# Performance work log

Hardware: AMD Instinct MI355X
Metric: run time of the kernel (lower is better)

Reference implementation:

```python
import jax, jax.numpy as jnp
import numpy as np

B, T, I = 16384, 50, 5
H = 128
PRED_LEN = 12


def _uniform(key, shape, bound):
    return jax.random.uniform(key, shape, jnp.float32, -bound, bound)


def setup_inputs() -> dict:
    key = jax.random.key(0)
    ks = jax.random.split(key, 12)
    bound = 1.0 / np.sqrt(H)  # PyTorch LSTM/Linear default init
    return {
        "x": jax.random.normal(ks[0], (B, T, I), jnp.float32),
        "enc_Wih": _uniform(ks[1], (4 * H, I), bound),
        "enc_Whh": _uniform(ks[2], (4 * H, H), bound),
        "enc_bih": _uniform(ks[3], (4 * H,), bound),
        "enc_bhh": _uniform(ks[4], (4 * H,), bound),
        "dec_Wih": _uniform(ks[5], (4 * H, I), bound),
        "dec_Whh": _uniform(ks[6], (4 * H, H), bound),
        "dec_bih": _uniform(ks[7], (4 * H,), bound),
        "dec_bhh": _uniform(ks[8], (4 * H,), bound),
        "lin_W": _uniform(ks[9], (2, H), bound),
        "lin_b": _uniform(ks[10], (2,), bound),
    }


def _lstm_cell(x_t, h, c, Wih, Whh, bih, bhh):
    # PyTorch gate order: i, f, g, o
    gates = x_t @ Wih.T + h @ Whh.T + (bih + bhh)  # [B, 4H]
    i, f, g, o = jnp.split(gates, 4, axis=-1)
    i = jax.nn.sigmoid(i)
    f = jax.nn.sigmoid(f)
    g = jnp.tanh(g)
    o = jax.nn.sigmoid(o)
    c_new = f * c + i * g
    h_new = o * jnp.tanh(c_new)
    return h_new, c_new


def reference(x, enc_Wih, enc_Whh, enc_bih, enc_bhh,
              dec_Wih, dec_Whh, dec_bih, dec_bhh, lin_W, lin_b):
    b = x.shape[0]
    h0 = jnp.zeros((b, H), x.dtype)
    c0 = jnp.zeros((b, H), x.dtype)

    # ---- encoder LSTM over the history sequence ----
    def enc_step(carry, x_t):
        h, c = carry
        h, c = _lstm_cell(x_t, h, c, enc_Wih, enc_Whh, enc_bih, enc_bhh)
        return (h, c), None

    (h, c), _ = jax.lax.scan(enc_step, (h0, c0), jnp.swapaxes(x, 0, 1))

    static_context = x[:, -1, 2:]          # [B, I-2]
    last_velocity = x[:, -1, :2]           # [B, 2]
    dec_in0 = jnp.concatenate([last_velocity, static_context], axis=1)  # [B, I]

    def dec_step(carry, _):
        h, c, dec_in = carry
        h, c = _lstm_cell(dec_in, h, c, dec_Wih, dec_Whh, dec_bih, dec_bhh)
        pred = h @ lin_W.T + lin_b                      # [B, 2]
        dec_in = jnp.concatenate([pred, static_context], axis=1)
        return (h, c, dec_in), pred

    _, preds = jax.lax.scan(dec_step, (h, c, dec_in0), None, length=PRED_LEN)
    return jnp.swapaxes(preds, 0, 1)  # [B, pred_len, 2]
```

## Files before the change

kernel.cpp:

```cpp
#include <hip/hip_runtime.h>
#include <cstdint>

#define TT 50
#define II 5
#define PRED 12

typedef _Float16 f16;
typedef _Float16 f16x8 __attribute__((ext_vector_type(8)));
typedef float f32x4 __attribute__((ext_vector_type(4)));

#define K1 1.4426950408889634f
#define K2 2.8853900817779268f

__device__ __forceinline__ float cellact(float xi, float xf, float xg, float xo, float& c) {
    float ea = __builtin_amdgcn_exp2f(xi * -K1);
    float ef = __builtin_amdgcn_exp2f(xf * -K1);
    float eg = __builtin_amdgcn_exp2f(xg *  K2);
    float eo = __builtin_amdgcn_exp2f(xo * -K1);
    float a1 = 1.f + ea, a2 = 1.f + ef, a3 = eg + 1.f, a4 = eg - 1.f;
    float t1 = a1 * a3;
    float cn = fmaf(c, t1, a4 * a2) * __builtin_amdgcn_rcpf(t1 * a2);
    c = cn;
    float cc = fminf(fmaxf(cn, -15.f), 15.f);
    float ec = __builtin_amdgcn_exp2f(cc * K2);
    return (ec - 1.f) * __builtin_amdgcn_rcpf((1.f + eo) * (ec + 1.f));
}

__device__ __forceinline__ void load_weights(const float* __restrict__ Wih, const float* __restrict__ Whh,
                                             const float* __restrict__ bih, const float* __restrict__ bhh,
                                             f16x8 wr[4][5], int w, int cl, int q) {
    #pragma unroll
    for (int gs = 0; gs < 4; ++gs) {
        const int g = gs * 128 + w * 16 + cl;
        const float* row = Whh + g * 128 + q * 8;
        #pragma unroll
        for (int kc = 0; kc < 4; ++kc) {
            float4 a = *(const float4*)(row + kc * 32);
            float4 b = *(const float4*)(row + kc * 32 + 4);
            f16x8 r;
            r[0] = (f16)a.x; r[1] = (f16)a.y; r[2] = (f16)a.z; r[3] = (f16)a.w;
            r[4] = (f16)b.x; r[5] = (f16)b.y; r[6] = (f16)b.z; r[7] = (f16)b.w;
            wr[gs][kc] = r;
        }
        f16x8 r;
        #pragma unroll
        for (int j = 0; j < 8; ++j) {
            int k = 128 + q * 8 + j;
            float v = 0.f;
            if (k < 133)       v = Wih[g * 5 + (k - 128)];
            else if (k == 133) v = bih[g] + bhh[g];
            r[j] = (f16)v;
        }
        wr[gs][4] = r;
    }
}

__device__ __forceinline__ void do_mfma(const unsigned char* sb, const f16x8 wr[4][5],
                                        f32x4 acc[4][2], int cl, int q) {
    #pragma unroll
    for (int ns = 0; ns < 2; ++ns) {
        const int srow = ns * 16 + cl;
        #pragma unroll
        for (int kc = 0; kc < 5; ++kc) {
            const int phys = (kc * 4 + q) ^ (2 * cl);
            f16x8 bf = *(const f16x8*)(sb + srow * 512 + phys * 16);
            acc[0][ns] = __builtin_amdgcn_mfma_f32_16x16x32_f16(wr[0][kc], bf, acc[0][ns], 0, 0, 0);
            acc[1][ns] = __builtin_amdgcn_mfma_f32_16x16x32_f16(wr[1][kc], bf, acc[1][ns], 0, 0, 0);
            acc[2][ns] = __builtin_amdgcn_mfma_f32_16x16x32_f16(wr[2][kc], bf, acc[2][ns], 0, 0, 0);
            acc[3][ns] = __builtin_amdgcn_mfma_f32_16x16x32_f16(wr[3][kc], bf, acc[3][ns], 0, 0, 0);
        }
    }
}

__device__ __forceinline__ void do_act(f32x4 acc[4][2], float creg[2][4], unsigned char* dst,
                                       int cl, int physh, int hoff) {
    #pragma unroll
    for (int ns = 0; ns < 2; ++ns) {
        union { f16 h[4]; uint2 u; } pk;
        #pragma unroll
        for (int idx = 0; idx < 4; ++idx)
            pk.h[idx] = (f16)cellact(acc[0][ns][idx], acc[1][ns][idx], acc[2][ns][idx],
                                     acc[3][ns][idx], creg[ns][idx]);
        *(uint2*)(dst + (ns * 16 + cl) * 512 + physh * 16 + hoff) = pk.u;
    }
}

__device__ __forceinline__ void do_act_dec(f32x4 acc[4][2], float creg[2][4], unsigned char* dst,
                                           int cl, int physh, int hoff,
                                           const float w0r[4], const float w1r[4],
                                           float p0[2], float p1[2]) {
    #pragma unroll
    for (int ns = 0; ns < 2; ++ns) {
        union { f16 h[4]; uint2 u; } pk;
        p0[ns] = 0.f; p1[ns] = 0.f;
        #pragma unroll
        for (int idx = 0; idx < 4; ++idx) {
            float hv = cellact(acc[0][ns][idx], acc[1][ns][idx], acc[2][ns][idx],
                               acc[3][ns][idx], creg[ns][idx]);
            p0[ns] = fmaf(hv, w0r[idx], p0[ns]);
            p1[ns] = fmaf(hv, w1r[idx], p1[ns]);
            pk.h[idx] = (f16)hv;
        }
        *(uint2*)(dst + (ns * 16 + cl) * 512 + physh * 16 + hoff) = pk.u;
    }
}

__device__ __forceinline__ void write_x5(unsigned char* sb, int sl,
                                         float v0, float v1, float v2, float v3, float v4) {
    union { f16 h[8]; uint4 u; } pk;
    pk.h[0] = (f16)v0; pk.h[1] = (f16)v1; pk.h[2] = (f16)v2;
    pk.h[3] = (f16)v3; pk.h[4] = (f16)v4;
    pk.h[5] = (f16)1.f; pk.h[6] = (f16)0.f; pk.h[7] = (f16)0.f;
    int phys = 16 ^ (2 * (sl & 15));
    *(uint4*)(sb + sl * 512 + phys * 16) = pk.u;
}

__global__ __launch_bounds__(512, 2)
void lstm_kernel(const float* __restrict__ x,
                 const float* __restrict__ eWih, const float* __restrict__ eWhh,
                 const float* __restrict__ ebih, const float* __restrict__ ebhh,
                 const float* __restrict__ dWih, const float* __restrict__ dWhh,
                 const float* __restrict__ dbih, const float* __restrict__ dbhh,
                 const float* __restrict__ linW, const float* __restrict__ linB,
                 float* __restrict__ out) {
    __shared__ __align__(16) unsigned char stateA[2][32 * 512];
    __shared__ __align__(16) unsigned char stateB[2][32 * 512];
    __shared__ float ppA[8][32][2], ppB[8][32][2];

    const int tid  = threadIdx.x;
    const int lane = tid & 63;
    const int w    = tid >> 6;
    const int q    = lane >> 4;
    const int cl   = lane & 15;
    const int s0   = blockIdx.x * 64;
    const int jb   = w * 16 + q * 4;
    const int physh = ((jb >> 3) ^ (2 * cl)) & 31;
    const int hoff  = (jb & 7) * 2;

    f16x8 wr[4][5];
    load_weights(eWih, eWhh, ebih, ebhh, wr, w, cl, q);

    {
        uint4 z{0, 0, 0, 0};
        uint4* pa = (uint4*)&stateA[0][0];
        uint4* pb = (uint4*)&stateB[0][0];
        #pragma unroll
        for (int r = 0; r < 4; ++r) { pa[tid + r * 512] = z; pb[tid + r * 512] = z; }
    }
    float cregA[2][4], cregB[2][4];
    #pragma unroll
    for (int a = 0; a < 2; ++a)
        #pragma unroll
        for (int b = 0; b < 4; ++b) { cregA[a][b] = 0.f; cregB[a][b] = 0.f; }
    f32x4 accA[4][2], accB[4][2];
    const f32x4 z4 = {0.f, 0.f, 0.f, 0.f};

    __syncthreads();
    if (tid < 32) {
        const float* xr = x + (size_t)(s0 + tid) * (TT * II);
        write_x5(stateA[0], tid, xr[0], xr[1], xr[2], xr[3], xr[4]);
    }
    __syncthreads();

    #pragma unroll 1
    for (int t = 0; t < TT; ++t) {
        unsigned char* curA = stateA[t & 1];
        unsigned char* nxtA = stateA[(t + 1) & 1];
        unsigned char* curB = stateB[t & 1];
        float xv0 = 0, xv1 = 0, xv2 = 0, xv3 = 0, xv4 = 0;
        if (tid < 64) {
            int tl = (tid < 32) ? ((t < TT - 1) ? t + 1 : TT - 1) : t;
            const float* xr = x + (size_t)(s0 + tid) * (TT * II) + tl * II;
            xv0 = xr[0]; xv1 = xr[1]; xv2 = xr[2]; xv3 = xr[3]; xv4 = xr[4];
        }
        #pragma unroll
        for (int gs = 0; gs < 4; ++gs) { accA[gs][0] = z4; accA[gs][1] = z4; }
        do_mfma(curA, wr, accA, cl, q);
        if (t > 0) do_act(accB, cregB, curB, cl, physh, hoff);
        if (tid >= 32 && tid < 64) write_x5(curB, tid - 32, xv0, xv1, xv2, xv3, xv4);
        __syncthreads();
        #pragma unroll
        for (int gs = 0; gs < 4; ++gs) { accB[gs][0] = z4; accB[gs][1] = z4; }
        do_mfma(curB, wr, accB, cl, q);
        do_act(accA, cregA, nxtA, cl, physh, hoff);
        if (tid < 32) write_x5(nxtA, tid, xv0, xv1, xv2, xv3, xv4);
        __syncthreads();
    }
    do_act(accB, cregB, stateB[0], cl, physh, hoff);
    if (tid >= 32 && tid < 64) {
        const float* xr = x + (size_t)(s0 + tid) * (TT * II) + (TT - 1) * II;
        write_x5(stateB[0], tid - 32, xr[0], xr[1], xr[2], xr[3], xr[4]);
    }
    __syncthreads();

    load_weights(dWih, dWhh, dbih, dbhh, wr, w, cl, q);
    float w0r[4], w1r[4];
    #pragma unroll
    for (int idx = 0; idx < 4; ++idx) {
        w0r[idx] = linW[jb + idx];
        w1r[idx] = linW[128 + jb + idx];
    }
    float sc0 = 0, sc1 = 0, sc2 = 0, lb0 = 0, lb1 = 0;
    if (tid < 64) {
        const float* xr = x + (size_t)(s0 + tid) * (TT * II) + (TT - 1) * II;
        sc0 = xr[2]; sc1 = xr[3]; sc2 = xr[4];
        lb0 = linB[0]; lb1 = linB[1];
    }

    #pragma unroll 1
    for (int dt = 0; dt < PRED; ++dt) {
        int t = TT + dt;
        unsigned char* curA = stateA[t & 1]; unsigned char* nxtA = stateA[(t + 1) & 1];
        unsigned char* curB = stateB[t & 1]; unsigned char* nxtB = stateB[(t + 1) & 1];
        #pragma unroll
        for (int gs = 0; gs < 4; ++gs) {
            accA[gs][0] = z4; accA[gs][1] = z4;
            accB[gs][0] = z4; accB[gs][1] = z4;
        }
        do_mfma(curA, wr, accA, cl, q);
        do_mfma(curB, wr, accB, cl, q);
        float p0A[2], p1A[2], p0B[2], p1B[2];
        do_act_dec(accA, cregA, nxtA, cl, physh, hoff, w0r, w1r, p0A, p1A);
        do_act_dec(accB, cregB, nxtB, cl, physh, hoff, w0r, w1r, p0B, p1B);
        #pragma unroll
        for (int ns = 0; ns < 2; ++ns) {
            p0A[ns] += __shfl_xor(p0A[ns], 16); p0A[ns] += __shfl_xor(p0A[ns], 32);
            p1A[ns] += __shfl_xor(p1A[ns], 16); p1A[ns] += __shfl_xor(p1A[ns], 32);
            p0B[ns] += __shfl_xor(p0B[ns], 16); p0B[ns] += __shfl_xor(p0B[ns], 32);
            p1B[ns] += __shfl_xor(p1B[ns], 16); p1B[ns] += __shfl_xor(p1B[ns], 32);
        }
        if (q == 0) {
            #pragma unroll
            for (int ns = 0; ns < 2; ++ns) {
                ppA[w][ns * 16 + cl][0] = p0A[ns]; ppA[w][ns * 16 + cl][1] = p1A[ns];
                ppB[w][ns * 16 + cl][0] = p0B[ns]; ppB[w][ns * 16 + cl][1] = p1B[ns];
            }
        }
        __syncthreads();
        if (tid < 64) {
            int sl = tid & 31;
            float (*pp)[32][2] = (tid < 32) ? ppA : ppB;
            float a0 = lb0, a1 = lb1;
            #pragma unroll
            for (int ww = 0; ww < 8; ++ww) { a0 += pp[ww][sl][0]; a1 += pp[ww][sl][1]; }
            float2 o2; o2.x = a0; o2.y = a1;
            *(float2*)(out + (size_t)(s0 + tid) * (PRED * 2) + dt * 2) = o2;
            write_x5((tid < 32) ? nxtA : nxtB, sl, a0, a1, sc0, sc1, sc2);
        }
        __syncthreads();
    }
}

extern "C" void kernel_launch(void* const* d_in, const int* in_sizes, int n_in,
                              void* d_out, int out_size, void* d_ws, size_t ws_size,
                              hipStream_t stream) {
    (void)in_sizes; (void)n_in; (void)out_size; (void)d_ws; (void)ws_size;
    const float* x    = (const float*)d_in[0];
    const float* eWih = (const float*)d_in[1];
    const float* eWhh = (const float*)d_in[2];
    const float* ebih = (const float*)d_in[3];
    const float* ebhh = (const float*)d_in[4];
    const float* dWih = (const float*)d_in[5];
    const float* dWhh = (const float*)d_in[6];
    const float* dbih = (const float*)d_in[7];
    const float* dbhh = (const float*)d_in[8];
    const float* linW = (const float*)d_in[9];
    const float* linB = (const float*)d_in[10];

    lstm_kernel<<<256, 512, 0, stream>>>(x, eWih, eWhh, ebih, ebhh,
                                         dWih, dWhh, dbih, dbhh,
                                         linW, linB, (float*)d_out);
}
```

Baseline: 290.6 us.

## Restructure encoder ping-pong pipeline and interleave MFMA with activations via sched_group_barrier

Reorders the encoder loop so both half-tiles start together: A's first MFMA is issued before the loop, and each half-iteration then pairs one tile's MFMA with the other tile's activation, with a peeled final step. It adds sched_group_barrier hints that interleave MFMA, LDS reads, transcendental and VALU instructions, so matrix work overlaps the gate math in both encoder and decoder. The aim is to hide activation latency behind MFMA throughput, at the cost of a more fragile schedule and a wrong instruction mix if the group counts do not match the real code.

```diff
diff --git a/kernel.cpp b/kernel.cpp
--- a/kernel.cpp
+++ b/kernel.cpp
@@ -26,6 +26,25 @@
     return (ec - 1.f) * __builtin_amdgcn_rcpf((1.f + eo) * (ec + 1.f));
 }
 
+__device__ __forceinline__ void sched_enc() {
+    #pragma unroll
+    for (int i = 0; i < 8; ++i) {
+        __builtin_amdgcn_sched_group_barrier(0x100, 2, 0);
+        __builtin_amdgcn_sched_group_barrier(0x008, 5, 0);
+        __builtin_amdgcn_sched_group_barrier(0x400, 7, 0);
+        __builtin_amdgcn_sched_group_barrier(0x002, 20, 0);
+    }
+}
+__device__ __forceinline__ void sched_dec() {
+    #pragma unroll
+    for (int i = 0; i < 16; ++i) {
+        __builtin_amdgcn_sched_group_barrier(0x100, 2, 0);
+        __builtin_amdgcn_sched_group_barrier(0x008, 5, 0);
+        __builtin_amdgcn_sched_group_barrier(0x400, 7, 0);
+        __builtin_amdgcn_sched_group_barrier(0x002, 20, 0);
+    }
+}
+
 __device__ __forceinline__ void load_weights(const float* __restrict__ Wih, const float* __restrict__ Whh,
                                              const float* __restrict__ bih, const float* __restrict__ bhh,
                                              f16x8 wr[4][5], int w, int cl, int q) {
@@ -156,41 +175,57 @@
     const f32x4 z4 = {0.f, 0.f, 0.f, 0.f};
 
     __syncthreads();
-    if (tid < 32) {
+    if (tid < 64) {
         const float* xr = x + (size_t)(s0 + tid) * (TT * II);
-        write_x5(stateA[0], tid, xr[0], xr[1], xr[2], xr[3], xr[4]);
-    }
+        write_x5((tid < 32) ? stateA[0] : stateB[0], tid & 31,
+                 xr[0], xr[1], xr[2], xr[3], xr[4]);
+    }
+    __syncthreads();
+
+    #pragma unroll
+    for (int gs = 0; gs < 4; ++gs) { accA[gs][0] = z4; accA[gs][1] = z4; }
+    do_mfma(stateA[0], wr, accA, cl, q);
     __syncthreads();
 
     #pragma unroll 1
-    for (int t = 0; t < TT; ++t) {
-        unsigned char* curA = stateA[t & 1];
-        unsigned char* nxtA = stateA[(t + 1) & 1];
-        unsigned char* curB = stateB[t & 1];
+    for (int t = 0; t < TT - 1; ++t) {
         float xv0 = 0, xv1 = 0, xv2 = 0, xv3 = 0, xv4 = 0;
         if (tid < 64) {
-            int tl = (tid < 32) ? ((t < TT - 1) ? t + 1 : TT - 1) : t;
-            const float* xr = x + (size_t)(s0 + tid) * (TT * II) + tl * II;
+            const float* xr = x + (size_t)(s0 + tid) * (TT * II) + (t + 1) * II;
             xv0 = xr[0]; xv1 = xr[1]; xv2 = xr[2]; xv3 = xr[3]; xv4 = xr[4];
         }
-        #pragma unroll
-        for (int gs = 0; gs < 4; ++gs) { accA[gs][0] = z4; accA[gs][1] = z4; }
-        do_mfma(curA, wr, accA, cl, q);
-        if (t > 0) do_act(accB, cregB, curB, cl, physh, hoff);
-        if (tid >= 32 && tid < 64) write_x5(curB, tid - 32, xv0, xv1, xv2, xv3, xv4);
-        __syncthreads();
+        unsigned char* curB = stateB[t & 1];
+        unsigned char* nxtA = stateA[(t + 1) & 1];
+        unsigned char* nxtB = stateB[(t + 1) & 1];
         #pragma unroll
         for (int gs = 0; gs < 4; ++gs) { accB[gs][0] = z4; accB[gs][1] = z4; }
         do_mfma(curB, wr, accB, cl, q);
         do_act(accA, cregA, nxtA, cl, physh, hoff);
         if (tid < 32) write_x5(nxtA, tid, xv0, xv1, xv2, xv3, xv4);
+        sched_enc();
         __syncthreads();
-    }
+        #pragma unroll
+        for (int gs = 0; gs < 4; ++gs) { accA[gs][0] = z4; accA[gs][1] = z4; }
+        do_mfma(nxtA, wr, accA, cl, q);
+        do_act(accB, cregB, nxtB, cl, physh, hoff);
+        if (tid >= 32 && tid < 64) write_x5(nxtB, tid - 32, xv0, xv1, xv2, xv3, xv4);
+        sched_enc();
+        __syncthreads();
+    }
+    float xv0 = 0, xv1 = 0, xv2 = 0, xv3 = 0, xv4 = 0;
+    if (tid < 64) {
+        const float* xr = x + (size_t)(s0 + tid) * (TT * II) + (TT - 1) * II;
+        xv0 = xr[0]; xv1 = xr[1]; xv2 = xr[2]; xv3 = xr[3]; xv4 = xr[4];
+    }
+    #pragma unroll
+    for (int gs = 0; gs < 4; ++gs) { accB[gs][0] = z4; accB[gs][1] = z4; }
+    do_mfma(stateB[1], wr, accB, cl, q);
+    do_act(accA, cregA, stateA[0], cl, physh, hoff);
+    if (tid < 32) write_x5(stateA[0], tid, xv0, xv1, xv2, xv3, xv4);
+    sched_enc();
+    __syncthreads();
     do_act(accB, cregB, stateB[0], cl, physh, hoff);
-    if (tid >= 32 && tid < 64) {
-        const float* xr = x + (size_t)(s0 + tid) * (TT * II) + (TT - 1) * II;
-        write_x5(stateB[0], tid - 32, xr[0], xr[1], xr[2], xr[3], xr[4]);
-    }
+    if (tid >= 32 && tid < 64) write_x5(stateB[0], tid - 32, xv0, xv1, xv2, xv3, xv4);
     __syncthreads();
 
     load_weights(dWih, dWhh, dbih, dbhh, wr, w, cl, q);
@@ -200,12 +235,8 @@
         w0r[idx] = linW[jb + idx];
         w1r[idx] = linW[128 + jb + idx];
     }
-    float sc0 = 0, sc1 = 0, sc2 = 0, lb0 = 0, lb1 = 0;
-    if (tid < 64) {
-        const float* xr = x + (size_t)(s0 + tid) * (TT * II) + (TT - 1) * II;
-        sc0 = xr[2]; sc1 = xr[3]; sc2 = xr[4];
-        lb0 = linB[0]; lb1 = linB[1];
-    }
+    float sc0 = xv2, sc1 = xv3, sc2 = xv4, lb0 = 0, lb1 = 0;
+    if (tid < 64) { lb0 = linB[0]; lb1 = linB[1]; }
 
     #pragma unroll 1
     for (int dt = 0; dt < PRED; ++dt) {
@@ -222,6 +253,7 @@
         float p0A[2], p1A[2], p0B[2], p1B[2];
         do_act_dec(accA, cregA, nxtA, cl, physh, hoff, w0r, w1r, p0A, p1A);
         do_act_dec(accB, cregB, nxtB, cl, physh, hoff, w0r, w1r, p0B, p1B);
+        sched_dec();
         #pragma unroll
         for (int ns = 0; ns < 2; ++ns) {
             p0A[ns] += __shfl_xor(p0A[ns], 16); p0A[ns] += __shfl_xor(p0A[ns], 32);
```

Result: no change. 289.0 us (-0.6%).

## Specialize waves into MFMA producers and activation consumers via shared gate buffers

Applied to the files above, without the earlier changes.

Splits each block's eight waves into four MFMA waves, which each hold eight gate row tiles of weights, and four activation waves that read fp32 gates from a swizzled shared buffer and apply the cell update. Two 16-sample groups alternate so matrix and activation work overlap across the two halves. Block size drops from 64 to 32 samples and the grid doubles. This adds fp32 gate traffic through LDS and makes the MFMA waves hold twice as many weight registers, which may cost occupancy.

```diff
diff --git a/kernel.cpp b/kernel.cpp
--- a/kernel.cpp
+++ b/kernel.cpp
@@ -26,85 +26,6 @@
     return (ec - 1.f) * __builtin_amdgcn_rcpf((1.f + eo) * (ec + 1.f));
 }
 
-__device__ __forceinline__ void load_weights(const float* __restrict__ Wih, const float* __restrict__ Whh,
-                                             const float* __restrict__ bih, const float* __restrict__ bhh,
-                                             f16x8 wr[4][5], int w, int cl, int q) {
-    #pragma unroll
-    for (int gs = 0; gs < 4; ++gs) {
-        const int g = gs * 128 + w * 16 + cl;
-        const float* row = Whh + g * 128 + q * 8;
-        #pragma unroll
-        for (int kc = 0; kc < 4; ++kc) {
-            float4 a = *(const float4*)(row + kc * 32);
-            float4 b = *(const float4*)(row + kc * 32 + 4);
-            f16x8 r;
-            r[0] = (f16)a.x; r[1] = (f16)a.y; r[2] = (f16)a.z; r[3] = (f16)a.w;
-            r[4] = (f16)b.x; r[5] = (f16)b.y; r[6] = (f16)b.z; r[7] = (f16)b.w;
-            wr[gs][kc] = r;
-        }
-        f16x8 r;
-        #pragma unroll
-        for (int j = 0; j < 8; ++j) {
-            int k = 128 + q * 8 + j;
-            float v = 0.f;
-            if (k < 133)       v = Wih[g * 5 + (k - 128)];
-            else if (k == 133) v = bih[g] + bhh[g];
-            r[j] = (f16)v;
-        }
-        wr[gs][4] = r;
-    }
-}
-
-__device__ __forceinline__ void do_mfma(const unsigned char* sb, const f16x8 wr[4][5],
-                                        f32x4 acc[4][2], int cl, int q) {
-    #pragma unroll
-    for (int ns = 0; ns < 2; ++ns) {
-        const int srow = ns * 16 + cl;
-        #pragma unroll
-        for (int kc = 0; kc < 5; ++kc) {
-            const int phys = (kc * 4 + q) ^ (2 * cl);
-            f16x8 bf = *(const f16x8*)(sb + srow * 512 + phys * 16);
-            acc[0][ns] = __builtin_amdgcn_mfma_f32_16x16x32_f16(wr[0][kc], bf, acc[0][ns], 0, 0, 0);
-            acc[1][ns] = __builtin_amdgcn_mfma_f32_16x16x32_f16(wr[1][kc], bf, acc[1][ns], 0, 0, 0);
-            acc[2][ns] = __builtin_amdgcn_mfma_f32_16x16x32_f16(wr[2][kc], bf, acc[2][ns], 0, 0, 0);
-            acc[3][ns] = __builtin_amdgcn_mfma_f32_16x16x32_f16(wr[3][kc], bf, acc[3][ns], 0, 0, 0);
-        }
-    }
-}
-
-__device__ __forceinline__ void do_act(f32x4 acc[4][2], float creg[2][4], unsigned char* dst,
-                                       int cl, int physh, int hoff) {
-    #pragma unroll
-    for (int ns = 0; ns < 2; ++ns) {
-        union { f16 h[4]; uint2 u; } pk;
-        #pragma unroll
-        for (int idx = 0; idx < 4; ++idx)
-            pk.h[idx] = (f16)cellact(acc[0][ns][idx], acc[1][ns][idx], acc[2][ns][idx],
-                                     acc[3][ns][idx], creg[ns][idx]);
-        *(uint2*)(dst + (ns * 16 + cl) * 512 + physh * 16 + hoff) = pk.u;
-    }
-}
-
-__device__ __forceinline__ void do_act_dec(f32x4 acc[4][2], float creg[2][4], unsigned char* dst,
-                                           int cl, int physh, int hoff,
-                                           const float w0r[4], const float w1r[4],
-                                           float p0[2], float p1[2]) {
-    #pragma unroll
-    for (int ns = 0; ns < 2; ++ns) {
-        union { f16 h[4]; uint2 u; } pk;
-        p0[ns] = 0.f; p1[ns] = 0.f;
-        #pragma unroll
-        for (int idx = 0; idx < 4; ++idx) {
-            float hv = cellact(acc[0][ns][idx], acc[1][ns][idx], acc[2][ns][idx],
-                               acc[3][ns][idx], creg[ns][idx]);
-            p0[ns] = fmaf(hv, w0r[idx], p0[ns]);
-            p1[ns] = fmaf(hv, w1r[idx], p1[ns]);
-            pk.h[idx] = (f16)hv;
-        }
-        *(uint2*)(dst + (ns * 16 + cl) * 512 + physh * 16 + hoff) = pk.u;
-    }
-}
-
 __device__ __forceinline__ void write_x5(unsigned char* sb, int sl,
                                          float v0, float v1, float v2, float v3, float v4) {
     union { f16 h[8]; uint4 u; } pk;
@@ -115,6 +36,71 @@
     *(uint4*)(sb + sl * 512 + phys * 16) = pk.u;
 }
 
+__device__ __forceinline__ void load_weights8(const float* __restrict__ Wih,
+                                              const float* __restrict__ Whh,
+                                              const float* __restrict__ bih,
+                                              const float* __restrict__ bhh,
+                                              f16x8 (&wr)[8][5], int mw, int cl, int q) {
+    #pragma unroll
+    for (int r = 0; r < 8; ++r) {
+        int g = (mw * 8 + r) * 16 + cl;
+        const float* row = Whh + g * 128 + q * 8;
+        #pragma unroll
+        for (int kc = 0; kc < 4; ++kc) {
+            float4 a = *(const float4*)(row + kc * 32);
+            float4 b = *(const float4*)(row + kc * 32 + 4);
+            f16x8 t;
+            t[0] = (f16)a.x; t[1] = (f16)a.y; t[2] = (f16)a.z; t[3] = (f16)a.w;
+            t[4] = (f16)b.x; t[5] = (f16)b.y; t[6] = (f16)b.z; t[7] = (f16)b.w;
+            wr[r][kc] = t;
+        }
+        f16x8 t;
+        #pragma unroll
+        for (int j = 0; j < 8; ++j) {
+            int k = 128 + q * 8 + j;
+            float v = 0.f;
+            if (k < 133)       v = Wih[g * 5 + (k - 128)];
+            else if (k == 133) v = bih[g] + bhh[g];
+            t[j] = (f16)v;
+        }
+        wr[r][4] = t;
+    }
+}
+
+__device__ __forceinline__ void mfma_gates(const unsigned char* sbuf, float* gbuf,
+                                           const f16x8 (&wr)[8][5], int mw, int cl, int q) {
+    f32x4 acc[8];
+    #pragma unroll
+    for (int r = 0; r < 8; ++r) acc[r] = (f32x4){0.f, 0.f, 0.f, 0.f};
+    #pragma unroll
+    for (int kc = 0; kc < 5; ++kc) {
+        int phys = (kc * 4 + q) ^ (2 * cl);
+        f16x8 bf = *(const f16x8*)(sbuf + cl * 512 + phys * 16);
+        #pragma unroll
+        for (int r = 0; r < 8; ++r)
+            acc[r] = __builtin_amdgcn_mfma_f32_16x16x32_f16(wr[r][kc], bf, acc[r], 0, 0, 0);
+    }
+    unsigned char* grow = (unsigned char*)gbuf + cl * 2048;
+    #pragma unroll
+    for (int r = 0; r < 8; ++r) {
+        int ch = (mw * 8 + r) * 4 + q;
+        *(f32x4*)(grow + ((ch ^ (cl & 7)) * 16)) = acc[r];
+    }
+}
+
+__device__ __forceinline__ void read_gates(const float* gbuf, int sloc, int j0,
+                                           float (&gv)[4][8]) {
+    const unsigned char* grow = (const unsigned char*)gbuf + sloc * 2048;
+    #pragma unroll
+    for (int tix = 0; tix < 4; ++tix) {
+        int c0 = tix * 32 + (j0 >> 2);
+        f32x4 a = *(const f32x4*)(grow + ((c0 ^ (sloc & 7)) * 16));
+        f32x4 b = *(const f32x4*)(grow + (((c0 + 1) ^ (sloc & 7)) * 16));
+        gv[tix][0] = a[0]; gv[tix][1] = a[1]; gv[tix][2] = a[2]; gv[tix][3] = a[3];
+        gv[tix][4] = b[0]; gv[tix][5] = b[1]; gv[tix][6] = b[2]; gv[tix][7] = b[3];
+    }
+}
+
 __global__ __launch_bounds__(512, 2)
 void lstm_kernel(const float* __restrict__ x,
                  const float* __restrict__ eWih, const float* __restrict__ eWhh,
@@ -123,131 +109,217 @@
                  const float* __restrict__ dbih, const float* __restrict__ dbhh,
                  const float* __restrict__ linW, const float* __restrict__ linB,
                  float* __restrict__ out) {
-    __shared__ __align__(16) unsigned char stateA[2][32 * 512];
-    __shared__ __align__(16) unsigned char stateB[2][32 * 512];
-    __shared__ float ppA[8][32][2], ppB[8][32][2];
+    __shared__ __align__(16) unsigned char stateA[16 * 512];
+    __shared__ __align__(16) unsigned char stateB[16 * 512];
+    __shared__ __align__(16) float gatesA[16 * 512];
+    __shared__ __align__(16) float gatesB[16 * 512];
+    __shared__ float pp[2][2][4][16][2];
 
     const int tid  = threadIdx.x;
     const int lane = tid & 63;
     const int w    = tid >> 6;
     const int q    = lane >> 4;
     const int cl   = lane & 15;
-    const int s0   = blockIdx.x * 64;
-    const int jb   = w * 16 + q * 4;
-    const int physh = ((jb >> 3) ^ (2 * cl)) & 31;
-    const int hoff  = (jb & 7) * 2;
-
-    f16x8 wr[4][5];
-    load_weights(eWih, eWhh, ebih, ebhh, wr, w, cl, q);
+    const int s0   = blockIdx.x * 32;
+    const bool mf  = (w < 4);
+    const int mw   = w;
+    const int u    = w - 4;
+    const int j0   = u * 32 + q * 8;
+    const int physh = (u * 4 + q) ^ (2 * cl);
+
+    f16x8 wr[8][5];
+    float creg[2][8];
+    #pragma unroll
+    for (int a = 0; a < 2; ++a)
+        #pragma unroll
+        for (int b = 0; b < 8; ++b) creg[a][b] = 0.f;
+    float w0r[8], w1r[8];
+    float velA0 = 0, velA1 = 0, scA0 = 0, scA1 = 0, scA2 = 0;
+    float velB0 = 0, velB1 = 0, scB0 = 0, scB1 = 0, scB2 = 0;
+    float lb0 = 0, lb1 = 0;
+
+    if (mf) load_weights8(eWih, eWhh, ebih, ebhh, wr, mw, cl, q);
 
     {
         uint4 z{0, 0, 0, 0};
-        uint4* pa = (uint4*)&stateA[0][0];
-        uint4* pb = (uint4*)&stateB[0][0];
-        #pragma unroll
-        for (int r = 0; r < 4; ++r) { pa[tid + r * 512] = z; pb[tid + r * 512] = z; }
-    }
-    float cregA[2][4], cregB[2][4];
-    #pragma unroll
-    for (int a = 0; a < 2; ++a)
-        #pragma unroll
-        for (int b = 0; b < 4; ++b) { cregA[a][b] = 0.f; cregB[a][b] = 0.f; }
-    f32x4 accA[4][2], accB[4][2];
-    const f32x4 z4 = {0.f, 0.f, 0.f, 0.f};
-
-    __syncthreads();
-    if (tid < 32) {
-        const float* xr = x + (size_t)(s0 + tid) * (TT * II);
-        write_x5(stateA[0], tid, xr[0], xr[1], xr[2], xr[3], xr[4]);
-    }
+        ((uint4*)stateA)[tid] = z;
+        ((uint4*)stateB)[tid] = z;
+    }
+    __syncthreads();
+    if ((w == 4 || w == 5) && lane < 16) {
+        int sg = s0 + (w - 4) * 16 + lane;
+        const float* xr = x + (size_t)sg * (TT * II);
+        write_x5((w == 4) ? stateA : stateB, lane, xr[0], xr[1], xr[2], xr[3], xr[4]);
+    }
+    __syncthreads();
+    if (mf) mfma_gates(stateA, gatesA, wr, mw, cl, q);
     __syncthreads();
 
     #pragma unroll 1
-    for (int t = 0; t < TT; ++t) {
-        unsigned char* curA = stateA[t & 1];
-        unsigned char* nxtA = stateA[(t + 1) & 1];
-        unsigned char* curB = stateB[t & 1];
-        float xv0 = 0, xv1 = 0, xv2 = 0, xv3 = 0, xv4 = 0;
-        if (tid < 64) {
-            int tl = (tid < 32) ? ((t < TT - 1) ? t + 1 : TT - 1) : t;
-            const float* xr = x + (size_t)(s0 + tid) * (TT * II) + tl * II;
-            xv0 = xr[0]; xv1 = xr[1]; xv2 = xr[2]; xv3 = xr[3]; xv4 = xr[4];
-        }
-        #pragma unroll
-        for (int gs = 0; gs < 4; ++gs) { accA[gs][0] = z4; accA[gs][1] = z4; }
-        do_mfma(curA, wr, accA, cl, q);
-        if (t > 0) do_act(accB, cregB, curB, cl, physh, hoff);
-        if (tid >= 32 && tid < 64) write_x5(curB, tid - 32, xv0, xv1, xv2, xv3, xv4);
+    for (int t = 0; t < TT - 1; ++t) {
+        if (mf) {
+            mfma_gates(stateB, gatesB, wr, mw, cl, q);
+        } else {
+            float xv0 = 0, xv1 = 0, xv2 = 0, xv3 = 0, xv4 = 0;
+            if (w == 4 && lane < 16) {
+                const float* xr = x + (size_t)(s0 + lane) * (TT * II) + (t + 1) * II;
+                xv0 = xr[0]; xv1 = xr[1]; xv2 = xr[2]; xv3 = xr[3]; xv4 = xr[4];
+            }
+            float gv[4][8];
+            read_gates(gatesA, cl, j0, gv);
+            union { f16 h[8]; uint4 uu; } pk;
+            #pragma unroll
+            for (int jj = 0; jj < 8; ++jj)
+                pk.h[jj] = (f16)cellact(gv[0][jj], gv[1][jj], gv[2][jj], gv[3][jj], creg[0][jj]);
+            *(uint4*)(stateA + cl * 512 + physh * 16) = pk.uu;
+            if (w == 4 && lane < 16) write_x5(stateA, lane, xv0, xv1, xv2, xv3, xv4);
+        }
         __syncthreads();
-        #pragma unroll
-        for (int gs = 0; gs < 4; ++gs) { accB[gs][0] = z4; accB[gs][1] = z4; }
-        do_mfma(curB, wr, accB, cl, q);
-        do_act(accA, cregA, nxtA, cl, physh, hoff);
-        if (tid < 32) write_x5(nxtA, tid, xv0, xv1, xv2, xv3, xv4);
+        if (mf) {
+            mfma_gates(stateA, gatesA, wr, mw, cl, q);
+        } else {
+            float xv0 = 0, xv1 = 0, xv2 = 0, xv3 = 0, xv4 = 0;
+            if (w == 5 && lane < 16) {
+                const float* xr = x + (size_t)(s0 + 16 + lane) * (TT * II) + (t + 1) * II;
+                xv0 = xr[0]; xv1 = xr[1]; xv2 = xr[2]; xv3 = xr[3]; xv4 = xr[4];
+            }
+            float gv[4][8];
+            read_gates(gatesB, cl, j0, gv);
+            union { f16 h[8]; uint4 uu; } pk;
+            #pragma unroll
+            for (int jj = 0; jj < 8; ++jj)
+                pk.h[jj] = (f16)cellact(gv[0][jj], gv[1][jj], gv[2][jj], gv[3][jj], creg[1][jj]);
+            *(uint4*)(stateB + cl * 512 + physh * 16) = pk.uu;
+            if (w == 5 && lane < 16) write_x5(stateB, lane, xv0, xv1, xv2, xv3, xv4);
+        }
         __syncthreads();
     }
-    do_act(accB, cregB, stateB[0], cl, physh, hoff);
-    if (tid >= 32 && tid < 64) {
-        const float* xr = x + (size_t)(s0 + tid) * (TT * II) + (TT - 1) * II;
-        write_x5(stateB[0], tid - 32, xr[0], xr[1], xr[2], xr[3], xr[4]);
-    }
-    __syncthreads();
-
-    load_weights(dWih, dWhh, dbih, dbhh, wr, w, cl, q);
-    float w0r[4], w1r[4];
-    #pragma unroll
-    for (int idx = 0; idx < 4; ++idx) {
-        w0r[idx] = linW[jb + idx];
-        w1r[idx] = linW[128 + jb + idx];
-    }
-    float sc0 = 0, sc1 = 0, sc2 = 0, lb0 = 0, lb1 = 0;
-    if (tid < 64) {
-        const float* xr = x + (size_t)(s0 + tid) * (TT * II) + (TT - 1) * II;
-        sc0 = xr[2]; sc1 = xr[3]; sc2 = xr[4];
+    if (mf) {
+        mfma_gates(stateB, gatesB, wr, mw, cl, q);
+    } else {
+        float gv[4][8];
+        read_gates(gatesA, cl, j0, gv);
+        union { f16 h[8]; uint4 uu; } pk;
+        #pragma unroll
+        for (int jj = 0; jj < 8; ++jj)
+            pk.h[jj] = (f16)cellact(gv[0][jj], gv[1][jj], gv[2][jj], gv[3][jj], creg[0][jj]);
+        *(uint4*)(stateA + cl * 512 + physh * 16) = pk.uu;
+    }
+    __syncthreads();
+    if (mf) {
+        load_weights8(dWih, dWhh, dbih, dbhh, wr, mw, cl, q);
+        const float* xeA = x + (size_t)(s0 + cl) * (TT * II) + (TT - 1) * II;
+        velA0 = xeA[0]; velA1 = xeA[1]; scA0 = xeA[2]; scA1 = xeA[3]; scA2 = xeA[4];
+        const float* xeB = x + (size_t)(s0 + 16 + cl) * (TT * II) + (TT - 1) * II;
+        velB0 = xeB[0]; velB1 = xeB[1]; scB0 = xeB[2]; scB1 = xeB[3]; scB2 = xeB[4];
         lb0 = linB[0]; lb1 = linB[1];
-    }
+    } else {
+        float gv[4][8];
+        read_gates(gatesB, cl, j0, gv);
+        union { f16 h[8]; uint4 uu; } pk;
+        #pragma unroll
+        for (int jj = 0; jj < 8; ++jj)
+            pk.h[jj] = (f16)cellact(gv[0][jj], gv[1][jj], gv[2][jj], gv[3][jj], creg[1][jj]);
+        *(uint4*)(stateB + cl * 512 + physh * 16) = pk.uu;
+        #pragma unroll
+        for (int jj = 0; jj < 8; ++jj) {
+            w0r[jj] = linW[j0 + jj];
+            w1r[jj] = linW[128 + j0 + jj];
+        }
+    }
+    __syncthreads();
+    if (mf) {
+        if (q == 0) write_x5(stateA, cl, velA0, velA1, scA0, scA1, scA2);
+        mfma_gates(stateA, gatesA, wr, mw, cl, q);
+    }
+    __syncthreads();
 
     #pragma unroll 1
-    for (int dt = 0; dt < PRED; ++dt) {
-        int t = TT + dt;
-        unsigned char* curA = stateA[t & 1]; unsigned char* nxtA = stateA[(t + 1) & 1];
-        unsigned char* curB = stateB[t & 1]; unsigned char* nxtB = stateB[(t + 1) & 1];
-        #pragma unroll
-        for (int gs = 0; gs < 4; ++gs) {
-            accA[gs][0] = z4; accA[gs][1] = z4;
-            accB[gs][0] = z4; accB[gs][1] = z4;
-        }
-        do_mfma(curA, wr, accA, cl, q);
-        do_mfma(curB, wr, accB, cl, q);
-        float p0A[2], p1A[2], p0B[2], p1B[2];
-        do_act_dec(accA, cregA, nxtA, cl, physh, hoff, w0r, w1r, p0A, p1A);
-        do_act_dec(accB, cregB, nxtB, cl, physh, hoff, w0r, w1r, p0B, p1B);
-        #pragma unroll
-        for (int ns = 0; ns < 2; ++ns) {
-            p0A[ns] += __shfl_xor(p0A[ns], 16); p0A[ns] += __shfl_xor(p0A[ns], 32);
-            p1A[ns] += __shfl_xor(p1A[ns], 16); p1A[ns] += __shfl_xor(p1A[ns], 32);
-            p0B[ns] += __shfl_xor(p0B[ns], 16); p0B[ns] += __shfl_xor(p0B[ns], 32);
-            p1B[ns] += __shfl_xor(p1B[ns], 16); p1B[ns] += __shfl_xor(p1B[ns], 32);
-        }
-        if (q == 0) {
-            #pragma unroll
-            for (int ns = 0; ns < 2; ++ns) {
-                ppA[w][ns * 16 + cl][0] = p0A[ns]; ppA[w][ns * 16 + cl][1] = p1A[ns];
-                ppB[w][ns * 16 + cl][0] = p0B[ns]; ppB[w][ns * 16 + cl][1] = p1B[ns];
+    for (int d = 0; d < PRED; ++d) {
+        if (mf) {
+            float p0, p1;
+            if (d == 0) { p0 = velB0; p1 = velB1; }
+            else {
+                int pr = (d - 1) & 1;
+                p0 = lb0; p1 = lb1;
+                #pragma unroll
+                for (int uu = 0; uu < 4; ++uu) {
+                    p0 += pp[1][pr][uu][cl][0];
+                    p1 += pp[1][pr][uu][cl][1];
+                }
+                if (mw == 0 && q == 0) {
+                    float2 o2; o2.x = p0; o2.y = p1;
+                    *(float2*)(out + (size_t)(s0 + 16 + cl) * (PRED * 2) + (d - 1) * 2) = o2;
+                }
+            }
+            if (q == 0) write_x5(stateB, cl, p0, p1, scB0, scB1, scB2);
+            mfma_gates(stateB, gatesB, wr, mw, cl, q);
+        } else {
+            float gv[4][8];
+            read_gates(gatesA, cl, j0, gv);
+            union { f16 h[8]; uint4 uu; } pk;
+            float np0 = 0.f, np1 = 0.f;
+            #pragma unroll
+            for (int jj = 0; jj < 8; ++jj) {
+                float hv = cellact(gv[0][jj], gv[1][jj], gv[2][jj], gv[3][jj], creg[0][jj]);
+                np0 = fmaf(hv, w0r[jj], np0);
+                np1 = fmaf(hv, w1r[jj], np1);
+                pk.h[jj] = (f16)hv;
+            }
+            *(uint4*)(stateA + cl * 512 + physh * 16) = pk.uu;
+            np0 += __shfl_xor(np0, 16); np0 += __shfl_xor(np0, 32);
+            np1 += __shfl_xor(np1, 16); np1 += __shfl_xor(np1, 32);
+            if (lane < 16) {
+                pp[0][d & 1][u][cl][0] = np0;
+                pp[0][d & 1][u][cl][1] = np1;
             }
         }
         __syncthreads();
-        if (tid < 64) {
-            int sl = tid & 31;
-            float (*pp)[32][2] = (tid < 32) ? ppA : ppB;
-            float a0 = lb0, a1 = lb1;
-            #pragma unroll
-            for (int ww = 0; ww < 8; ++ww) { a0 += pp[ww][sl][0]; a1 += pp[ww][sl][1]; }
-            float2 o2; o2.x = a0; o2.y = a1;
-            *(float2*)(out + (size_t)(s0 + tid) * (PRED * 2) + dt * 2) = o2;
-            write_x5((tid < 32) ? nxtA : nxtB, sl, a0, a1, sc0, sc1, sc2);
+        if (mf) {
+            int pr = d & 1;
+            float p0 = lb0, p1 = lb1;
+            #pragma unroll
+            for (int uu = 0; uu < 4; ++uu) {
+                p0 += pp[0][pr][uu][cl][0];
+                p1 += pp[0][pr][uu][cl][1];
+            }
+            if (mw == 0 && q == 0) {
+                float2 o2; o2.x = p0; o2.y = p1;
+                *(float2*)(out + (size_t)(s0 + cl) * (PRED * 2) + d * 2) = o2;
+            }
+            if (q == 0) write_x5(stateA, cl, p0, p1, scA0, scA1, scA2);
+            mfma_gates(stateA, gatesA, wr, mw, cl, q);
+        } else {
+            float gv[4][8];
+            read_gates(gatesB, cl, j0, gv);
+            union { f16 h[8]; uint4 uu; } pk;
+            float np0 = 0.f, np1 = 0.f;
+            #pragma unroll
+            for (int jj = 0; jj < 8; ++jj) {
+                float hv = cellact(gv[0][jj], gv[1][jj], gv[2][jj], gv[3][jj], creg[1][jj]);
+                np0 = fmaf(hv, w0r[jj], np0);
+                np1 = fmaf(hv, w1r[jj], np1);
+                pk.h[jj] = (f16)hv;
+            }
+            *(uint4*)(stateB + cl * 512 + physh * 16) = pk.uu;
+            np0 += __shfl_xor(np0, 16); np0 += __shfl_xor(np0, 32);
+            np1 += __shfl_xor(np1, 16); np1 += __shfl_xor(np1, 32);
+            if (lane < 16) {
+                pp[1][d & 1][u][cl][0] = np0;
+                pp[1][d & 1][u][cl][1] = np1;
+            }
         }
         __syncthreads();
+    }
+    if (mf && mw == 0 && q == 0) {
+        float p0 = lb0, p1 = lb1;
+        #pragma unroll
+        for (int uu = 0; uu < 4; ++uu) {
+            p0 += pp[1][(PRED - 1) & 1][uu][cl][0];
+            p1 += pp[1][(PRED - 1) & 1][uu][cl][1];
+        }
+        float2 o2; o2.x = p0; o2.y = p1;
+        *(float2*)(out + (size_t)(s0 + 16 + cl) * (PRED * 2) + (PRED - 1) * 2) = o2;
     }
 }
 
@@ -267,7 +339,7 @@
     const float* linW = (const float*)d_in[9];
     const float* linB = (const float*)d_in[10];
 
-    lstm_kernel<<<256, 512, 0, stream>>>(x, eWih, eWhh, ebih, ebhh,
+    lstm_kernel<<<512, 512, 0, stream>>>(x, eWih, eWhh, ebih, ebhh,
                                          dWih, dWhh, dbih, dbhh,
                                          linW, linB, (float*)d_out);
 }
```

Measured after the change: 548.2 us. +88.6%, slower.

## Shrink LSTM blocks to 16 sequences, 4 waves, drop A/B ping-pong pipelining

Applied to the files above, without the earlier changes.

Restructures the work split so that each block handles 16 sequences with 256 threads, and each wave owns two 16-row gate slices of the hidden units. This replaces the 64-sequence, 512-thread block that interleaved two 32-sequence halves to overlap MFMA with activations. The grid grows to 1024 blocks, each thread holds twice as many weight fragments in registers, and each B-fragment LDS load now feeds 8 MFMAs. The LDS swizzle also gains an extra xor term. In exchange, the explicit overlap of matrix work and activation math across the two halves is lost, and register pressure per thread rises.

```diff
diff --git a/kernel.cpp b/kernel.cpp
--- a/kernel.cpp
+++ b/kernel.cpp
@@ -26,83 +26,8 @@
     return (ec - 1.f) * __builtin_amdgcn_rcpf((1.f + eo) * (ec + 1.f));
 }
 
-__device__ __forceinline__ void load_weights(const float* __restrict__ Wih, const float* __restrict__ Whh,
-                                             const float* __restrict__ bih, const float* __restrict__ bhh,
-                                             f16x8 wr[4][5], int w, int cl, int q) {
-    #pragma unroll
-    for (int gs = 0; gs < 4; ++gs) {
-        const int g = gs * 128 + w * 16 + cl;
-        const float* row = Whh + g * 128 + q * 8;
-        #pragma unroll
-        for (int kc = 0; kc < 4; ++kc) {
-            float4 a = *(const float4*)(row + kc * 32);
-            float4 b = *(const float4*)(row + kc * 32 + 4);
-            f16x8 r;
-            r[0] = (f16)a.x; r[1] = (f16)a.y; r[2] = (f16)a.z; r[3] = (f16)a.w;
-            r[4] = (f16)b.x; r[5] = (f16)b.y; r[6] = (f16)b.z; r[7] = (f16)b.w;
-            wr[gs][kc] = r;
-        }
-        f16x8 r;
-        #pragma unroll
-        for (int j = 0; j < 8; ++j) {
-            int k = 128 + q * 8 + j;
-            float v = 0.f;
-            if (k < 133)       v = Wih[g * 5 + (k - 128)];
-            else if (k == 133) v = bih[g] + bhh[g];
-            r[j] = (f16)v;
-        }
-        wr[gs][4] = r;
-    }
-}
-
-__device__ __forceinline__ void do_mfma(const unsigned char* sb, const f16x8 wr[4][5],
-                                        f32x4 acc[4][2], int cl, int q) {
-    #pragma unroll
-    for (int ns = 0; ns < 2; ++ns) {
-        const int srow = ns * 16 + cl;
-        #pragma unroll
-        for (int kc = 0; kc < 5; ++kc) {
-            const int phys = (kc * 4 + q) ^ (2 * cl);
-            f16x8 bf = *(const f16x8*)(sb + srow * 512 + phys * 16);
-            acc[0][ns] = __builtin_amdgcn_mfma_f32_16x16x32_f16(wr[0][kc], bf, acc[0][ns], 0, 0, 0);
-            acc[1][ns] = __builtin_amdgcn_mfma_f32_16x16x32_f16(wr[1][kc], bf, acc[1][ns], 0, 0, 0);
-            acc[2][ns] = __builtin_amdgcn_mfma_f32_16x16x32_f16(wr[2][kc], bf, acc[2][ns], 0, 0, 0);
-            acc[3][ns] = __builtin_amdgcn_mfma_f32_16x16x32_f16(wr[3][kc], bf, acc[3][ns], 0, 0, 0);
-        }
-    }
-}
-
-__device__ __forceinline__ void do_act(f32x4 acc[4][2], float creg[2][4], unsigned char* dst,
-                                       int cl, int physh, int hoff) {
-    #pragma unroll
-    for (int ns = 0; ns < 2; ++ns) {
-        union { f16 h[4]; uint2 u; } pk;
-        #pragma unroll
-        for (int idx = 0; idx < 4; ++idx)
-            pk.h[idx] = (f16)cellact(acc[0][ns][idx], acc[1][ns][idx], acc[2][ns][idx],
-                                     acc[3][ns][idx], creg[ns][idx]);
-        *(uint2*)(dst + (ns * 16 + cl) * 512 + physh * 16 + hoff) = pk.u;
-    }
-}
-
-__device__ __forceinline__ void do_act_dec(f32x4 acc[4][2], float creg[2][4], unsigned char* dst,
-                                           int cl, int physh, int hoff,
-                                           const float w0r[4], const float w1r[4],
-                                           float p0[2], float p1[2]) {
-    #pragma unroll
-    for (int ns = 0; ns < 2; ++ns) {
-        union { f16 h[4]; uint2 u; } pk;
-        p0[ns] = 0.f; p1[ns] = 0.f;
-        #pragma unroll
-        for (int idx = 0; idx < 4; ++idx) {
-            float hv = cellact(acc[0][ns][idx], acc[1][ns][idx], acc[2][ns][idx],
-                               acc[3][ns][idx], creg[ns][idx]);
-            p0[ns] = fmaf(hv, w0r[idx], p0[ns]);
-            p1[ns] = fmaf(hv, w1r[idx], p1[ns]);
-            pk.h[idx] = (f16)hv;
-        }
-        *(uint2*)(dst + (ns * 16 + cl) * 512 + physh * 16 + hoff) = pk.u;
-    }
+__device__ __forceinline__ int swz(int ch, int sl) {
+    return ch ^ (2 * sl) ^ (sl >> 3);
 }
 
 __device__ __forceinline__ void write_x5(unsigned char* sb, int sl,
@@ -111,11 +36,57 @@
     pk.h[0] = (f16)v0; pk.h[1] = (f16)v1; pk.h[2] = (f16)v2;
     pk.h[3] = (f16)v3; pk.h[4] = (f16)v4;
     pk.h[5] = (f16)1.f; pk.h[6] = (f16)0.f; pk.h[7] = (f16)0.f;
-    int phys = 16 ^ (2 * (sl & 15));
-    *(uint4*)(sb + sl * 512 + phys * 16) = pk.u;
-}
-
-__global__ __launch_bounds__(512, 2)
+    *(uint4*)(sb + sl * 512 + swz(16, sl) * 16) = pk.u;
+}
+
+__device__ __forceinline__ void load_weights(const float* __restrict__ Wih,
+                                             const float* __restrict__ Whh,
+                                             const float* __restrict__ bih,
+                                             const float* __restrict__ bhh,
+                                             f16x8 (&wr)[4][2][5], int w, int cl, int q) {
+    #pragma unroll
+    for (int gs = 0; gs < 4; ++gs) {
+        #pragma unroll
+        for (int js = 0; js < 2; ++js) {
+            int g = (gs * 8 + w + 4 * js) * 16 + cl;
+            const float* row = Whh + g * 128 + q * 8;
+            #pragma unroll
+            for (int kc = 0; kc < 4; ++kc) {
+                float4 a = *(const float4*)(row + kc * 32);
+                float4 b = *(const float4*)(row + kc * 32 + 4);
+                f16x8 t;
+                t[0] = (f16)a.x; t[1] = (f16)a.y; t[2] = (f16)a.z; t[3] = (f16)a.w;
+                t[4] = (f16)b.x; t[5] = (f16)b.y; t[6] = (f16)b.z; t[7] = (f16)b.w;
+                wr[gs][js][kc] = t;
+            }
+            f16x8 t;
+            #pragma unroll
+            for (int j = 0; j < 8; ++j) {
+                int k = 128 + q * 8 + j;
+                float v = 0.f;
+                if (k < 133)       v = Wih[g * 5 + (k - 128)];
+                else if (k == 133) v = bih[g] + bhh[g];
+                t[j] = (f16)v;
+            }
+            wr[gs][js][4] = t;
+        }
+    }
+}
+
+__device__ __forceinline__ void do_mfma(const unsigned char* cur, const f16x8 (&wr)[4][2][5],
+                                        f32x4 (&acc)[4][2], int cl, int q) {
+    #pragma unroll
+    for (int kc = 0; kc < 5; ++kc) {
+        f16x8 bf = *(const f16x8*)(cur + cl * 512 + swz(kc * 4 + q, cl) * 16);
+        #pragma unroll
+        for (int gs = 0; gs < 4; ++gs)
+            #pragma unroll
+            for (int js = 0; js < 2; ++js)
+                acc[gs][js] = __builtin_amdgcn_mfma_f32_16x16x32_f16(wr[gs][js][kc], bf, acc[gs][js], 0, 0, 0);
+    }
+}
+
+__global__ __launch_bounds__(256, 2)
 void lstm_kernel(const float* __restrict__ x,
                  const float* __restrict__ eWih, const float* __restrict__ eWhh,
                  const float* __restrict__ ebih, const float* __restrict__ ebhh,
@@ -123,129 +94,121 @@
                  const float* __restrict__ dbih, const float* __restrict__ dbhh,
                  const float* __restrict__ linW, const float* __restrict__ linB,
                  float* __restrict__ out) {
-    __shared__ __align__(16) unsigned char stateA[2][32 * 512];
-    __shared__ __align__(16) unsigned char stateB[2][32 * 512];
-    __shared__ float ppA[8][32][2], ppB[8][32][2];
+    __shared__ __align__(16) unsigned char state[2][16 * 512];
+    __shared__ float pp[4][16][2];
 
     const int tid  = threadIdx.x;
     const int lane = tid & 63;
     const int w    = tid >> 6;
     const int q    = lane >> 4;
     const int cl   = lane & 15;
-    const int s0   = blockIdx.x * 64;
-    const int jb   = w * 16 + q * 4;
-    const int physh = ((jb >> 3) ^ (2 * cl)) & 31;
-    const int hoff  = (jb & 7) * 2;
-
-    f16x8 wr[4][5];
+    const int s0   = blockIdx.x * 16;
+
+    f16x8 wr[4][2][5];
     load_weights(eWih, eWhh, ebih, ebhh, wr, w, cl, q);
+
+    int physh[2], hoff = (q & 1) * 8;
+    #pragma unroll
+    for (int js = 0; js < 2; ++js)
+        physh[js] = swz((w + 4 * js) * 2 + (q >> 1), cl);
 
     {
         uint4 z{0, 0, 0, 0};
-        uint4* pa = (uint4*)&stateA[0][0];
-        uint4* pb = (uint4*)&stateB[0][0];
-        #pragma unroll
-        for (int r = 0; r < 4; ++r) { pa[tid + r * 512] = z; pb[tid + r * 512] = z; }
-    }
-    float cregA[2][4], cregB[2][4];
+        uint4* p = (uint4*)&state[0][0];
+        #pragma unroll
+        for (int r = 0; r < 4; ++r) p[tid + r * 256] = z;
+    }
+    float creg[2][4];
     #pragma unroll
     for (int a = 0; a < 2; ++a)
         #pragma unroll
-        for (int b = 0; b < 4; ++b) { cregA[a][b] = 0.f; cregB[a][b] = 0.f; }
-    f32x4 accA[4][2], accB[4][2];
+        for (int b = 0; b < 4; ++b) creg[a][b] = 0.f;
     const f32x4 z4 = {0.f, 0.f, 0.f, 0.f};
 
     __syncthreads();
-    if (tid < 32) {
+    if (tid < 16) {
         const float* xr = x + (size_t)(s0 + tid) * (TT * II);
-        write_x5(stateA[0], tid, xr[0], xr[1], xr[2], xr[3], xr[4]);
+        write_x5(state[0], tid, xr[0], xr[1], xr[2], xr[3], xr[4]);
     }
     __syncthreads();
 
     #pragma unroll 1
     for (int t = 0; t < TT; ++t) {
-        unsigned char* curA = stateA[t & 1];
-        unsigned char* nxtA = stateA[(t + 1) & 1];
-        unsigned char* curB = stateB[t & 1];
+        unsigned char* cur = state[t & 1];
+        unsigned char* nxt = state[(t + 1) & 1];
         float xv0 = 0, xv1 = 0, xv2 = 0, xv3 = 0, xv4 = 0;
-        if (tid < 64) {
-            int tl = (tid < 32) ? ((t < TT - 1) ? t + 1 : TT - 1) : t;
+        if (tid < 16) {
+            int tl = (t < TT - 1) ? t + 1 : TT - 1;
             const float* xr = x + (size_t)(s0 + tid) * (TT * II) + tl * II;
             xv0 = xr[0]; xv1 = xr[1]; xv2 = xr[2]; xv3 = xr[3]; xv4 = xr[4];
         }
-        #pragma unroll
-        for (int gs = 0; gs < 4; ++gs) { accA[gs][0] = z4; accA[gs][1] = z4; }
-        do_mfma(curA, wr, accA, cl, q);
-        if (t > 0) do_act(accB, cregB, curB, cl, physh, hoff);
-        if (tid >= 32 && tid < 64) write_x5(curB, tid - 32, xv0, xv1, xv2, xv3, xv4);
+        f32x4 acc[4][2];
+        #pragma unroll
+        for (int gs = 0; gs < 4; ++gs) { acc[gs][0] = z4; acc[gs][1] = z4; }
+        do_mfma(cur, wr, acc, cl, q);
+        #pragma unroll
+        for (int js = 0; js < 2; ++js) {
+            union { f16 h[4]; uint2 u; } pk;
+            #pragma unroll
+            for (int idx = 0; idx < 4; ++idx)
+                pk.h[idx] = (f16)cellact(acc[0][js][idx], acc[1][js][idx],
+                                         acc[2][js][idx], acc[3][js][idx], creg[js][idx]);
+            *(uint2*)(nxt + cl * 512 + physh[js] * 16 + hoff) = pk.u;
+        }
+        if (tid < 16) write_x5(nxt, tid, xv0, xv1, xv2, xv3, xv4);
         __syncthreads();
-        #pragma unroll
-        for (int gs = 0; gs < 4; ++gs) { accB[gs][0] = z4; accB[gs][1] = z4; }
-        do_mfma(curB, wr, accB, cl, q);
-        do_act(accA, cregA, nxtA, cl, physh, hoff);
-        if (tid < 32) write_x5(nxtA, tid, xv0, xv1, xv2, xv3, xv4);
-        __syncthreads();
-    }
-    do_act(accB, cregB, stateB[0], cl, physh, hoff);
-    if (tid >= 32 && tid < 64) {
-        const float* xr = x + (size_t)(s0 + tid) * (TT * II) + (TT - 1) * II;
-        write_x5(stateB[0], tid - 32, xr[0], xr[1], xr[2], xr[3], xr[4]);
-    }
-    __syncthreads();
+    }
 
     load_weights(dWih, dWhh, dbih, dbhh, wr, w, cl, q);
-    float w0r[4], w1r[4];
-    #pragma unroll
-    for (int idx = 0; idx < 4; ++idx) {
-        w0r[idx] = linW[jb + idx];
-        w1r[idx] = linW[128 + jb + idx];
-    }
+    float w0r[2][4], w1r[2][4];
+    #pragma unroll
+    for (int js = 0; js < 2; ++js)
+        #pragma unroll
+        for (int idx = 0; idx < 4; ++idx) {
+            int j = (w + 4 * js) * 16 + q * 4 + idx;
+            w0r[js][idx] = linW[j];
+            w1r[js][idx] = linW[128 + j];
+        }
     float sc0 = 0, sc1 = 0, sc2 = 0, lb0 = 0, lb1 = 0;
-    if (tid < 64) {
+    if (tid < 16) {
         const float* xr = x + (size_t)(s0 + tid) * (TT * II) + (TT - 1) * II;
         sc0 = xr[2]; sc1 = xr[3]; sc2 = xr[4];
         lb0 = linB[0]; lb1 = linB[1];
     }
 
     #pragma unroll 1
-    for (int dt = 0; dt < PRED; ++dt) {
-        int t = TT + dt;
-        unsigned char* curA = stateA[t & 1]; unsigned char* nxtA = stateA[(t + 1) & 1];
-        unsigned char* curB = stateB[t & 1]; unsigned char* nxtB = stateB[(t + 1) & 1];
-        #pragma unroll
-        for (int gs = 0; gs < 4; ++gs) {
-            accA[gs][0] = z4; accA[gs][1] = z4;
-            accB[gs][0] = z4; accB[gs][1] = z4;
-        }
-        do_mfma(curA, wr, accA, cl, q);
-        do_mfma(curB, wr, accB, cl, q);
-        float p0A[2], p1A[2], p0B[2], p1B[2];
-        do_act_dec(accA, cregA, nxtA, cl, physh, hoff, w0r, w1r, p0A, p1A);
-        do_act_dec(accB, cregB, nxtB, cl, physh, hoff, w0r, w1r, p0B, p1B);
-        #pragma unroll
-        for (int ns = 0; ns < 2; ++ns) {
-            p0A[ns] += __shfl_xor(p0A[ns], 16); p0A[ns] += __shfl_xor(p0A[ns], 32);
-            p1A[ns] += __shfl_xor(p1A[ns], 16); p1A[ns] += __shfl_xor(p1A[ns], 32);
-            p0B[ns] += __shfl_xor(p0B[ns], 16); p0B[ns] += __shfl_xor(p0B[ns], 32);
-            p1B[ns] += __shfl_xor(p1B[ns], 16); p1B[ns] += __shfl_xor(p1B[ns], 32);
-        }
-        if (q == 0) {
-            #pragma unroll
-            for (int ns = 0; ns < 2; ++ns) {
-                ppA[w][ns * 16 + cl][0] = p0A[ns]; ppA[w][ns * 16 + cl][1] = p1A[ns];
-                ppB[w][ns * 16 + cl][0] = p0B[ns]; ppB[w][ns * 16 + cl][1] = p1B[ns];
+    for (int d = 0; d < PRED; ++d) {
+        unsigned char* cur = state[d & 1];
+        unsigned char* nxt = state[(d + 1) & 1];
+        f32x4 acc[4][2];
+        #pragma unroll
+        for (int gs = 0; gs < 4; ++gs) { acc[gs][0] = z4; acc[gs][1] = z4; }
+        do_mfma(cur, wr, acc, cl, q);
+        float p0 = 0.f, p1 = 0.f;
+        #pragma unroll
+        for (int js = 0; js < 2; ++js) {
+            union { f16 h[4]; uint2 u; } pk;
+            #pragma unroll
+            for (int idx = 0; idx < 4; ++idx) {
+                float hv = cellact(acc[0][js][idx], acc[1][js][idx],
+                                   acc[2][js][idx], acc[3][js][idx], creg[js][idx]);
+                p0 = fmaf(hv, w0r[js][idx], p0);
+                p1 = fmaf(hv, w1r[js][idx], p1);
+                pk.h[idx] = (f16)hv;
             }
-        }
+            *(uint2*)(nxt + cl * 512 + physh[js] * 16 + hoff) = pk.u;
+        }
+        p0 += __shfl_xor(p0, 16); p0 += __shfl_xor(p0, 32);
+        p1 += __shfl_xor(p1, 16); p1 += __shfl_xor(p1, 32);
+        if (lane < 16) { pp[w][cl][0] = p0; pp[w][cl][1] = p1; }
         __syncthreads();
-        if (tid < 64) {
-            int sl = tid & 31;
-            float (*pp)[32][2] = (tid < 32) ? ppA : ppB;
+        if (tid < 16) {
             float a0 = lb0, a1 = lb1;
             #pragma unroll
-            for (int ww = 0; ww < 8; ++ww) { a0 += pp[ww][sl][0]; a1 += pp[ww][sl][1]; }
+            for (int ww = 0; ww < 4; ++ww) { a0 += pp[ww][tid][0]; a1 += pp[ww][tid][1]; }
             float2 o2; o2.x = a0; o2.y = a1;
-            *(float2*)(out + (size_t)(s0 + tid) * (PRED * 2) + dt * 2) = o2;
-            write_x5((tid < 32) ? nxtA : nxtB, sl, a0, a1, sc0, sc1, sc2);
+            *(float2*)(out + (size_t)(s0 + tid) * (PRED * 2) + d * 2) = o2;
+            write_x5(nxt, tid, a0, a1, sc0, sc1, sc2);
         }
         __syncthreads();
     }
@@ -267,7 +230,7 @@
     const float* linW = (const float*)d_in[9];
     const float* linB = (const float*)d_in[10];
 
-    lstm_kernel<<<256, 512, 0, stream>>>(x, eWih, eWhh, ebih, ebhh,
-                                         dWih, dWhh, dbih, dbhh,
-                                         linW, linB, (float*)d_out);
-}
+    lstm_kernel<<<1024, 256, 0, stream>>>(x, eWih, eWhh, ebih, ebhh,
+                                          dWih, dWhh, dbih, dbhh,
+                                          linW, linB, (float*)d_out);
+}
```

After: 421.3 us. 1.45x slower.
